# Kernel optimization log

Hardware: AMD Instinct MI355X
Metric: run time of the kernel (lower is better)

## Reference

```python
import jax, jax.numpy as jnp
from jax import lax
import numpy as np

DECAY = 0.5   # LIF membrane leak factor
VTH = 1.0     # firing threshold


def _conv(x, w, stride, pad):
    # x: [B,C,H,W], w: [O,I,kh,kw]
    return lax.conv_general_dilated(
        x, w, (stride, stride), [(pad, pad), (pad, pad)],
        dimension_numbers=('NCHW', 'OIHW', 'NCHW'))


def _convT(x, w, b, stride=2, pad=1):
    # torch ConvTranspose2d(in,out,k,stride,pad): w is [Cin,Cout,k,k]
    k = w.shape[-1]
    wf = jnp.flip(w, (-2, -1)).transpose(1, 0, 2, 3)  # -> [Cout,Cin,k,k]
    y = lax.conv_general_dilated(
        x, wf, (1, 1), [(k - 1 - pad, k - 1 - pad)] * 2,
        lhs_dilation=(stride, stride),
        dimension_numbers=('NCHW', 'OIHW', 'NCHW'))
    return y + b[None, :, None, None]


def setup_inputs() -> dict:
    key = jax.random.key(0)
    ks = jax.random.split(key, 8)
    T, B = 16, 32
    x_seq = (jax.random.uniform(ks[0], (T, B, 1, 100, 368)) < 0.1).astype(jnp.float32)

    def p(k, shape, fan_in):
        return jax.random.normal(k, shape, jnp.float32) * (1.0 / np.sqrt(fan_in))

    return {
        'x_seq': x_seq,
        'w1': p(ks[1], (16, 1, 5, 5), 25),
        'w2': p(ks[2], (32, 16, 3, 3), 16 * 9),
        'wd': p(ks[3], (64, 32, 3, 3), 32 * 9),
        'bd': jnp.zeros((64,), jnp.float32),
        'wt1': p(ks[4], (64, 32, 4, 4), 64 * 16),
        'bt1': jnp.zeros((32,), jnp.float32),
        'wt2': p(ks[5], (32, 2, 4, 4), 32 * 16),
        'bt2': jnp.zeros((2,), jnp.float32),
        'actual_batch_size': 32,
    }


def reference(x_seq, w1, w2, wd, bd, wt1, bt1, wt2, bt2, actual_batch_size):
    B = x_seq.shape[1]
    dt = x_seq.dtype
    mem1 = jnp.zeros((B, 16, 50, 184), dt)
    mem2 = jnp.zeros((B, 32, 25, 92), dt)

    def step(carry, x):
        m1, m2 = carry
        # spiking conv layer 1: leaky integrate, fire, hard reset
        m1 = m1 * DECAY + _conv(x, w1, 2, 2)
        s1 = (m1 >= VTH).astype(dt)
        m1 = m1 * (1.0 - s1)
        # spiking conv layer 2 (return_dense -> membrane kept for decoder)
        m2 = m2 * DECAY + _conv(s1, w2, 2, 1)
        s2 = (m2 >= VTH).astype(dt)
        m2 = m2 * (1.0 - s2)
        return (m1, m2), None

    (mem1, mem2), _ = lax.scan(step, (mem1, mem2), x_seq)

    # dense CNN decoder on final membrane state
    h = jax.nn.relu(_conv(mem2, wd, 1, 1) + bd[None, :, None, None])   # [B,64,25,92]
    h = jax.nn.relu(_convT(h, wt1, bt1))                               # [B,32,50,184]
    out = jax.nn.softplus(_convT(h, wt2, bt2))                         # [B,2,100,368]
    inv_tau_c_pred = out[:, 0:1]
    alpha_pred = out[:, 1:2]
    return inv_tau_c_pred, alpha_pred
```

## Files before the change

kernel.cpp:

```cpp
#include <hip/hip_runtime.h>
#include <hip/hip_bf16.h>
#include <cstddef>


#define T_STEPS 16
#define NB 32
#define H0 100
#define W0 368
#define C1 16
#define H1 50
#define W1 184
#define C2 32
#define H2 25
#define W2 92
#define CD 64
#define WPR 6
#define SITES2 2300
#define SITES1 9200

using f32x16 = __attribute__((ext_vector_type(16))) float;
using s16x8  = __attribute__((ext_vector_type(8))) short;

__device__ inline unsigned short f2bf(float f) {
    union { float f; unsigned int u; } v; v.f = f;
    unsigned int r = v.u + 0x7fffu + ((v.u >> 16) & 1u);
    return (unsigned short)(r >> 16);
}
__device__ inline float bf2f(unsigned short u) {
    union { unsigned int u; float f; } v; v.u = ((unsigned int)u) << 16;
    return v.f;
}
__device__ inline unsigned int pk2(float a, float b) {
    return (unsigned int)f2bf(a) | ((unsigned int)f2bf(b) << 16);
}
__device__ inline s16x8 ld8(const void* p) { return *reinterpret_cast<const s16x8*>(p); }

__global__ __launch_bounds__(256) void k_pack(const float* __restrict__ x,
                                              unsigned long long* __restrict__ xb) {
    long long gid = (long long)blockIdx.x * blockDim.x + threadIdx.x;
    long long widx = gid >> 6;
    int lane = (int)(gid & 63);
    const long long NWORDS = (long long)T_STEPS * NB * H0 * WPR;
    if (widx >= NWORDS) return;
    int wcol = (int)(widx % WPR);
    long long rowid = widx / WPR;
    int y = (int)(rowid % H0);
    long long tb = rowid / H0;
    int col = wcol * 64 + lane;
    float v = 0.f;
    if (col < W0) v = x[(tb * H0 + y) * W0 + col];
    unsigned long long mask = __ballot(v != 0.f);
    if (lane == 0) xb[widx] = mask;
}

__global__ __launch_bounds__(256) void k_snn1(const unsigned long long* __restrict__ xb,
                                              const float* __restrict__ w1,
                                              unsigned short* __restrict__ s1m) {
    __shared__ float sw[25 * C1];
    for (int i = threadIdx.x; i < 25 * C1; i += blockDim.x) {
        int k = i >> 4, c = i & 15;
        sw[i] = w1[c * 25 + k];
    }
    __syncthreads();

    int idx = blockIdx.x * blockDim.x + threadIdx.x;
    const int NPOS = NB * H1 * W1;
    if (idx >= NPOS) return;
    int x1 = idx % W1;
    int tmp = idx / W1;
    int y1 = tmp % H1;
    int b  = tmp / H1;

    float m1[C1];
#pragma unroll
    for (int c = 0; c < C1; ++c) m1[c] = 0.f;

    const int iy0 = 2 * y1 - 2;
    const int ix0 = 2 * x1 - 2;
    const int wi = ix0 >> 6;
    const int s  = ix0 & 63;

    for (int t = 0; t < T_STEPS; ++t) {
#pragma unroll
        for (int c = 0; c < C1; ++c) m1[c] *= 0.5f;

        const unsigned long long* xp = xb + ((size_t)(t * NB + b) * H0) * WPR;
        unsigned int bits25 = 0;
#pragma unroll
        for (int ky = 0; ky < 5; ++ky) {
            int iy = iy0 + ky;
            if (iy < 0 || iy >= H0) continue;
            const unsigned long long* row = xp + (size_t)iy * WPR;
            unsigned long long a = (wi >= 0) ? row[wi] : 0ull;
            unsigned long long bw = (wi + 1 < WPR) ? row[wi + 1] : 0ull;
            unsigned long long chunk = a >> s;
            if (s) chunk |= (bw << (64 - s));
            bits25 |= ((unsigned int)chunk & 31u) << (5 * ky);
        }
        while (bits25) {
            int k = __ffs(bits25) - 1;
            bits25 &= bits25 - 1;
            const float* wk = &sw[k * C1];
#pragma unroll
            for (int c = 0; c < C1; ++c) m1[c] += wk[c];
        }
        unsigned int mask = 0;
#pragma unroll
        for (int c = 0; c < C1; ++c) {
            if (m1[c] >= 1.0f) { mask |= (1u << c); m1[c] = 0.f; }
        }
        s1m[(size_t)t * NPOS + idx] = (unsigned short)mask;
    }
}

__global__ __launch_bounds__(256) void k_snn2(const unsigned short* __restrict__ s1m,
                                              const float* __restrict__ w2,
                                              unsigned short* __restrict__ mem2bf) {
    __shared__ float sw[9 * C1 * 36];
    for (int i = threadIdx.x; i < 9 * C1 * C2; i += blockDim.x) {
        int c2 = i & 31;
        int r = i >> 5;
        int ci = r & 15;
        int pos = r >> 4;
        sw[r * 36 + c2] = w2[(c2 * C1 + ci) * 9 + pos];
    }
    __syncthreads();

    int idx = blockIdx.x * blockDim.x + threadIdx.x;
    const int NPOS = NB * H2 * W2;
    if (idx >= NPOS) return;
    int x2 = idx % W2;
    int tmp = idx / W2;
    int y2 = tmp % H2;
    int b  = tmp / H2;

    float m2[C2];
#pragma unroll
    for (int c = 0; c < C2; ++c) m2[c] = 0.f;

    const int S1POS = NB * H1 * W1;
    for (int t = 0; t < T_STEPS; ++t) {
#pragma unroll
        for (int c = 0; c < C2; ++c) m2[c] *= 0.5f;
        const unsigned short* spk = s1m + (size_t)t * S1POS + (size_t)b * (H1 * W1);
#pragma unroll
        for (int ky = 0; ky < 3; ++ky) {
            int iy = 2 * y2 + ky - 1;
            if (iy < 0 || iy >= H1) continue;
#pragma unroll
            for (int kx = 0; kx < 3; ++kx) {
                int ix = 2 * x2 + kx - 1;
                if (ix < 0 || ix >= W1) continue;
                unsigned int mask = spk[iy * W1 + ix];
                while (mask) {
                    int ci = __ffs(mask) - 1;
                    mask &= mask - 1;
                    const float* wrow = &sw[((ky * 3 + kx) * C1 + ci) * 36];
#pragma unroll
                    for (int c = 0; c < C2; ++c) m2[c] += wrow[c];
                }
            }
        }
#pragma unroll
        for (int c = 0; c < C2; ++c) {
            if (m2[c] >= 1.0f) m2[c] = 0.f;
        }
    }
    size_t sbase = ((size_t)b * SITES2 + (size_t)y2 * W2 + x2) * C2;
    uint4* dst = (uint4*)(mem2bf + sbase);
#pragma unroll
    for (int g = 0; g < 4; ++g) {
        uint4 u;
        u.x = pk2(m2[g * 8 + 0], m2[g * 8 + 1]);
        u.y = pk2(m2[g * 8 + 2], m2[g * 8 + 3]);
        u.z = pk2(m2[g * 8 + 4], m2[g * 8 + 5]);
        u.w = pk2(m2[g * 8 + 6], m2[g * 8 + 7]);
        dst[g] = u;
    }
}

__global__ __launch_bounds__(256) void k_repackb(const float* __restrict__ wd,
                                                 const float* __restrict__ wt1,
                                                 const float* __restrict__ wt2,
                                                 unsigned short* __restrict__ wdb,
                                                 unsigned short* __restrict__ wt1b,
                                                 float* __restrict__ wt2k) {
    int gid = blockIdx.x * blockDim.x + threadIdx.x;
    if (gid < 64 * 288) {
        int co = gid / 288, k = gid % 288;
        int tap = k >> 5, ci = k & 31;
        wdb[gid] = f2bf(wd[((size_t)co * C2 + ci) * 9 + tap]);
    } else if (gid < 64 * 288 + 4 * 32 * 256) {
        int j = gid - 64 * 288;
        int par = j >> 13, co = (j >> 8) & 31, k = j & 255;
        int tap = k >> 6, ci = k & 63;
        int ty = tap >> 1, tx = tap & 1;
        int ry = par >> 1, rx = par & 1;
        int ky = ry ? (ty ? 0 : 2) : (ty ? 3 : 1);
        int kx = rx ? (tx ? 0 : 2) : (tx ? 3 : 1);
        wt1b[j] = f2bf(wt1[(((size_t)ci * 32 + co) * 4 + ky) * 4 + kx]);
    } else if (gid < 64 * 288 + 4 * 32 * 256 + 1024) {
        int j = gid - (64 * 288 + 4 * 32 * 256);
        int par = j >> 8, tap = (j >> 6) & 3, ci = (j >> 1) & 31, co = j & 1;
        int ty = tap >> 1, tx = tap & 1;
        int ry = par >> 1, rx = par & 1;
        int ky = ry ? (ty ? 0 : 2) : (ty ? 3 : 1);
        int kx = rx ? (tx ? 0 : 2) : (tx ? 3 : 1);
        wt2k[j] = wt2[(((size_t)ci * 2 + co) * 4 + ky) * 4 + kx];
    }
}

__global__ __launch_bounds__(256) void k_convd(const unsigned short* __restrict__ mem2bf,
                                               const unsigned short* __restrict__ wdb,
                                               const float* __restrict__ bd,
                                               unsigned short* __restrict__ h1bf) {
    int wave = threadIdx.x >> 6;
    int lane = threadIdx.x & 63;
    int col = lane & 31, hi = lane >> 5;
    int b = blockIdx.z;
    int n0 = (blockIdx.x * 4 + wave) * 32;
    int site = n0 + col;
    bool sval = site < SITES2;
    int sc = sval ? site : 0;
    int yy = sc / W2, xx = sc % W2;

    const char* ibase = (const char*)(mem2bf + (size_t)b * SITES2 * C2);
    int toff[9];
    bool tval[9];
#pragma unroll
    for (int ky = 0; ky < 3; ++ky)
#pragma unroll
        for (int kx = 0; kx < 3; ++kx) {
            int iy = yy + ky - 1, ix = xx + kx - 1;
            bool v = sval && iy >= 0 && iy < H2 && ix >= 0 && ix < W2;
            tval[ky * 3 + kx] = v;
            toff[ky * 3 + kx] = (iy * W2 + ix) * (C2 * 2);
        }

    const char* abase = (const char*)wdb;
    f32x16 acc0 = {}, acc1 = {};
    const s16x8 zero = {0, 0, 0, 0, 0, 0, 0, 0};
#pragma unroll
    for (int s = 0; s < 18; ++s) {
        int tap = s >> 1;
        int boff = (s & 1) * 32 + hi * 16;
        s16x8 bf = tval[tap] ? ld8(ibase + toff[tap] + boff) : zero;
        s16x8 a0 = ld8(abase + col * 576 + s * 32 + hi * 16);
        s16x8 a1 = ld8(abase + (col + 32) * 576 + s * 32 + hi * 16);
        acc0 = __builtin_amdgcn_mfma_f32_32x32x16_bf16(a0, bf, acc0, 0, 0, 0);
        acc1 = __builtin_amdgcn_mfma_f32_32x32x16_bf16(a1, bf, acc1, 0, 0, 0);
    }
    if (!sval) return;
    char* obase = (char*)(h1bf + ((size_t)b * SITES2 + site) * CD);
#pragma unroll
    for (int t = 0; t < 2; ++t) {
        const f32x16& ac = t ? acc1 : acc0;
#pragma unroll
        for (int q = 0; q < 4; ++q) {
            int co = t * 32 + 8 * q + 4 * hi;
            float v0 = fmaxf(ac[4 * q + 0] + bd[co + 0], 0.f);
            float v1 = fmaxf(ac[4 * q + 1] + bd[co + 1], 0.f);
            float v2 = fmaxf(ac[4 * q + 2] + bd[co + 2], 0.f);
            float v3 = fmaxf(ac[4 * q + 3] + bd[co + 3], 0.f);
            uint2 u; u.x = pk2(v0, v1); u.y = pk2(v2, v3);
            *(uint2*)(obase + co * 2) = u;
        }
    }
}

__global__ __launch_bounds__(256) void k_convt1(const unsigned short* __restrict__ h1bf,
                                                const unsigned short* __restrict__ wt1b,
                                                const float* __restrict__ bt1,
                                                unsigned short* __restrict__ h2bf) {
    int wave = threadIdx.x >> 6;
    int lane = threadIdx.x & 63;
    int col = lane & 31, hi = lane >> 5;
    int par = blockIdx.y;
    int ry = par >> 1, rx = par & 1;
    int b = blockIdx.z;
    int n0 = (blockIdx.x * 4 + wave) * 64;

    const char* ibase = (const char*)(h1bf + (size_t)b * SITES2 * CD);
    int toff[2][4];
    bool tval[2][4];
    int mm[2], nn[2];
    bool sv[2];
#pragma unroll
    for (int j = 0; j < 2; ++j) {
        int site = n0 + j * 32 + col;
        sv[j] = site < SITES2;
        int sc = sv[j] ? site : 0;
        int m = sc / W2, n = sc % W2;
        mm[j] = m; nn[j] = n;
        int iy1 = m + (ry ? 1 : -1);
        int ix1 = n + (rx ? 1 : -1);
        bool y1v = iy1 >= 0 && iy1 < H2;
        bool x1v = ix1 >= 0 && ix1 < W2;
#pragma unroll
        for (int t = 0; t < 4; ++t) {
            int ty = t >> 1, tx = t & 1;
            int iy = ty ? iy1 : m;
            int ix = tx ? ix1 : n;
            tval[j][t] = sv[j] && (ty ? y1v : true) && (tx ? x1v : true);
            toff[j][t] = (iy * W2 + ix) * (CD * 2);
        }
    }

    const char* abase = (const char*)(wt1b + (size_t)par * 32 * 256);
    f32x16 acc0 = {}, acc1 = {};
    const s16x8 zero = {0, 0, 0, 0, 0, 0, 0, 0};
#pragma unroll
    for (int s = 0; s < 16; ++s) {
        int tap = s >> 2;
        int boff = (s & 3) * 32 + hi * 16;
        s16x8 b0 = tval[0][tap] ? ld8(ibase + toff[0][tap] + boff) : zero;
        s16x8 b1 = tval[1][tap] ? ld8(ibase + toff[1][tap] + boff) : zero;
        s16x8 a = ld8(abase + col * 512 + s * 32 + hi * 16);
        acc0 = __builtin_amdgcn_mfma_f32_32x32x16_bf16(a, b0, acc0, 0, 0, 0);
        acc1 = __builtin_amdgcn_mfma_f32_32x32x16_bf16(a, b1, acc1, 0, 0, 0);
    }
#pragma unroll
    for (int j = 0; j < 2; ++j) {
        if (!sv[j]) continue;
        const f32x16& ac = j ? acc1 : acc0;
        int oy = 2 * mm[j] + ry, ox = 2 * nn[j] + rx;
        char* obase = (char*)(h2bf + ((size_t)b * SITES1 + (size_t)oy * W1 + ox) * C2);
#pragma unroll
        for (int q = 0; q < 4; ++q) {
            int co = 8 * q + 4 * hi;
            float v0 = fmaxf(ac[4 * q + 0] + bt1[co + 0], 0.f);
            float v1 = fmaxf(ac[4 * q + 1] + bt1[co + 1], 0.f);
            float v2 = fmaxf(ac[4 * q + 2] + bt1[co + 2], 0.f);
            float v3 = fmaxf(ac[4 * q + 3] + bt1[co + 3], 0.f);
            uint2 u; u.x = pk2(v0, v1); u.y = pk2(v2, v3);
            *(uint2*)(obase + co * 2) = u;
        }
    }
}

__global__ __launch_bounds__(256) void k_convt2(const unsigned short* __restrict__ h2bf,
                                                const float* __restrict__ wt2k,
                                                const float* __restrict__ bt2,
                                                float* __restrict__ out) {
    int i = blockIdx.x * blockDim.x + threadIdx.x;
    if (i >= SITES1) return;
    int par = blockIdx.y;
    int ry = par >> 1, rx = par & 1;
    int b = blockIdx.z;
    int m = i / W1, n = i % W1;
    int iy1 = m + (ry ? 1 : -1);
    int ix1 = n + (rx ? 1 : -1);
    bool y1v = iy1 >= 0 && iy1 < H1;
    bool x1v = ix1 >= 0 && ix1 < W1;

    float a0 = bt2[0], a1 = bt2[1];
    const unsigned short* ib = h2bf + (size_t)b * SITES1 * C2;
#pragma unroll
    for (int t = 0; t < 4; ++t) {
        int ty = t >> 1, tx = t & 1;
        if ((ty && !y1v) || (tx && !x1v)) continue;
        int iy = ty ? iy1 : m;
        int ix = tx ? ix1 : n;
        const unsigned short* p = ib + ((size_t)iy * W1 + ix) * C2;
        const float* w = wt2k + ((size_t)par * 4 + t) * 64;
#pragma unroll
        for (int g = 0; g < 4; ++g) {
            s16x8 v8 = ld8(p + g * 8);
#pragma unroll
            for (int e = 0; e < 8; ++e) {
                float v = bf2f((unsigned short)v8[e]);
                int ci = g * 8 + e;
                a0 += v * w[2 * ci];
                a1 += v * w[2 * ci + 1];
            }
        }
    }
    int oy = 2 * m + ry, ox = 2 * n + rx;
    size_t base_o = (size_t)b * (H0 * W0) + (size_t)oy * W0 + ox;
    out[base_o] = fmaxf(a0, 0.f) + log1pf(expf(-fabsf(a0)));
    out[(size_t)NB * H0 * W0 + base_o] = fmaxf(a1, 0.f) + log1pf(expf(-fabsf(a1)));
}

extern "C" void kernel_launch(void* const* d_in, const int* in_sizes, int n_in,
                              void* d_out, int out_size, void* d_ws, size_t ws_size,
                              hipStream_t stream) {
    const float* x   = (const float*)d_in[0];
    const float* w1  = (const float*)d_in[1];
    const float* w2  = (const float*)d_in[2];
    const float* wd  = (const float*)d_in[3];
    const float* bd  = (const float*)d_in[4];
    const float* wt1 = (const float*)d_in[5];
    const float* bt1 = (const float*)d_in[6];
    const float* wt2 = (const float*)d_in[7];
    const float* bt2 = (const float*)d_in[8];
    float* out = (float*)d_out;

    char* ws = (char*)d_ws;
    unsigned short* s1m    = (unsigned short*)(ws);
    unsigned short* mem2bf = (unsigned short*)(ws + 9420800);
    unsigned short* h1bf   = (unsigned short*)(ws + 14131200);
    unsigned short* h2bf   = (unsigned short*)(ws + 23552000);
    unsigned long long* xb = (unsigned long long*)(ws + 42393600);
    unsigned short* wdb    = (unsigned short*)(ws + 44851200);
    unsigned short* wt1b   = (unsigned short*)(ws + 44888064);
    float* wt2k            = (float*)(ws + 44953600);

    {
        long long nthreads = (long long)T_STEPS * NB * H0 * WPR * 64;
        int blocks = (int)((nthreads + 255) / 256);
        k_pack<<<blocks, 256, 0, stream>>>(x, xb);
    }
    {
        int n = NB * H1 * W1;
        k_snn1<<<(n + 255) / 256, 256, 0, stream>>>(xb, w1, s1m);
    }
    {
        int n = NB * H2 * W2;
        k_snn2<<<(n + 255) / 256, 256, 0, stream>>>(s1m, w2, mem2bf);
    }
    {
        int n = 64 * 288 + 4 * 32 * 256 + 1024;
        k_repackb<<<(n + 255) / 256, 256, 0, stream>>>(wd, wt1, wt2, wdb, wt1b, wt2k);
    }
    {
        dim3 g(18, 1, NB);
        k_convd<<<g, 256, 0, stream>>>(mem2bf, wdb, bd, h1bf);
    }
    {
        dim3 g(9, 4, NB);
        k_convt1<<<g, 256, 0, stream>>>(h1bf, wt1b, bt1, h2bf);
    }
    {
        dim3 g(36, 4, NB);
        k_convt2<<<g, 256, 0, stream>>>(h2bf, wt2k, bt2, out);
    }
}
```

Baseline: 230.7 us.

## Run SNN layer-2 spiking conv on MFMA with bf16x3 split weights and spike LUT

Replaces the per-thread sparse scalar accumulation in the second spiking conv layer with MFMA 32x32x16 bf16 matrix ops. Each 32-site tile's spike bitmasks are expanded into bf16 0/1 operands through a shared-memory lookup table. To keep fp32-level accuracy, the weights are split into three bf16 parts (hi, mid, lo) in the repack kernel, which now runs first. The membrane state stays in MFMA accumulators across timesteps. This trades the data-dependent bit-scan loops for dense matrix work, at the cost of 27 MFMAs per timestep and some rounding risk near the threshold.

```diff
diff --git a/kernel.cpp b/kernel.cpp
--- a/kernel.cpp
+++ b/kernel.cpp
@@ -114,77 +114,96 @@
 }
 
 __global__ __launch_bounds__(256) void k_snn2(const unsigned short* __restrict__ s1m,
-                                              const float* __restrict__ w2,
+                                              const unsigned short* __restrict__ w2b3,
                                               unsigned short* __restrict__ mem2bf) {
-    __shared__ float sw[9 * C1 * 36];
-    for (int i = threadIdx.x; i < 9 * C1 * C2; i += blockDim.x) {
-        int c2 = i & 31;
-        int r = i >> 5;
-        int ci = r & 15;
-        int pos = r >> 4;
-        sw[r * 36 + c2] = w2[(c2 * C1 + ci) * 9 + pos];
+    __shared__ uint4 lut[256];
+    {
+        int m = (int)threadIdx.x;
+        unsigned int wv[4];
+#pragma unroll
+        for (int h = 0; h < 4; ++h) {
+            unsigned int lo = (m >> (2 * h)) & 1u, hb = (m >> (2 * h + 1)) & 1u;
+            wv[h] = (lo ? 0x3F80u : 0u) | (hb ? 0x3F800000u : 0u);
+        }
+        lut[m] = make_uint4(wv[0], wv[1], wv[2], wv[3]);
     }
     __syncthreads();
 
-    int idx = blockIdx.x * blockDim.x + threadIdx.x;
-    const int NPOS = NB * H2 * W2;
-    if (idx >= NPOS) return;
-    int x2 = idx % W2;
-    int tmp = idx / W2;
-    int y2 = tmp % H2;
-    int b  = tmp / H2;
-
-    float m2[C2];
-#pragma unroll
-    for (int c = 0; c < C2; ++c) m2[c] = 0.f;
-
-    const int S1POS = NB * H1 * W1;
+    int wave = threadIdx.x >> 6;
+    int lane = threadIdx.x & 63;
+    int col = lane & 31, hi = lane >> 5;
+    int gsite = (blockIdx.x * 4 + wave) * 32 + col;
+    int b = gsite / SITES2;
+    int rest = gsite % SITES2;
+    int y2 = rest / W2, x2 = rest % W2;
+
+    int toff[9]; bool tval[9];
+#pragma unroll
+    for (int ky = 0; ky < 3; ++ky)
+#pragma unroll
+        for (int kx = 0; kx < 3; ++kx) {
+            int iy = 2 * y2 + ky - 1, ix = 2 * x2 + kx - 1;
+            tval[ky * 3 + kx] = iy >= 0 && iy < H1 && ix >= 0 && ix < W1;
+            toff[ky * 3 + kx] = iy * W1 + ix;
+        }
+
+    const char* ab = (const char*)w2b3;
+    s16x8 a0[9], a1[9], a2[9];
+#pragma unroll
+    for (int s = 0; s < 9; ++s) {
+        int ko = (s * 16 + hi * 8) * 2;
+        a0[s] = ld8(ab + (col * 144) * 2 + ko);
+        a1[s] = ld8(ab + ((32 + col) * 144) * 2 + ko);
+        a2[s] = ld8(ab + ((64 + col) * 144) * 2 + ko);
+    }
+
+    f32x16 acc = {};
+    int hsh = hi * 8;
+
     for (int t = 0; t < T_STEPS; ++t) {
-#pragma unroll
-        for (int c = 0; c < C2; ++c) m2[c] *= 0.5f;
-        const unsigned short* spk = s1m + (size_t)t * S1POS + (size_t)b * (H1 * W1);
-#pragma unroll
-        for (int ky = 0; ky < 3; ++ky) {
-            int iy = 2 * y2 + ky - 1;
-            if (iy < 0 || iy >= H1) continue;
-#pragma unroll
-            for (int kx = 0; kx < 3; ++kx) {
-                int ix = 2 * x2 + kx - 1;
-                if (ix < 0 || ix >= W1) continue;
-                unsigned int mask = spk[iy * W1 + ix];
-                while (mask) {
-                    int ci = __ffs(mask) - 1;
-                    mask &= mask - 1;
-                    const float* wrow = &sw[((ky * 3 + kx) * C1 + ci) * 36];
-#pragma unroll
-                    for (int c = 0; c < C2; ++c) m2[c] += wrow[c];
-                }
-            }
-        }
-#pragma unroll
-        for (int c = 0; c < C2; ++c) {
-            if (m2[c] >= 1.0f) m2[c] = 0.f;
-        }
-    }
-    size_t sbase = ((size_t)b * SITES2 + (size_t)y2 * W2 + x2) * C2;
-    uint4* dst = (uint4*)(mem2bf + sbase);
-#pragma unroll
-    for (int g = 0; g < 4; ++g) {
-        uint4 u;
-        u.x = pk2(m2[g * 8 + 0], m2[g * 8 + 1]);
-        u.y = pk2(m2[g * 8 + 2], m2[g * 8 + 3]);
-        u.z = pk2(m2[g * 8 + 4], m2[g * 8 + 5]);
-        u.w = pk2(m2[g * 8 + 6], m2[g * 8 + 7]);
-        dst[g] = u;
+        const unsigned short* spk = s1m + (size_t)t * (NB * H1 * W1) + (size_t)b * (H1 * W1);
+        unsigned int msk[9];
+#pragma unroll
+        for (int i = 0; i < 9; ++i)
+            msk[i] = tval[i] ? (unsigned int)spk[toff[i]] : 0u;
+
+#pragma unroll
+        for (int e = 0; e < 16; ++e) acc[e] *= 0.5f;
+
+#pragma unroll
+        for (int s = 0; s < 9; ++s) {
+            unsigned int byte = (msk[s] >> hsh) & 0xFFu;
+            s16x8 bf = *reinterpret_cast<const s16x8*>(&lut[byte]);
+            acc = __builtin_amdgcn_mfma_f32_32x32x16_bf16(a0[s], bf, acc, 0, 0, 0);
+            acc = __builtin_amdgcn_mfma_f32_32x32x16_bf16(a1[s], bf, acc, 0, 0, 0);
+            acc = __builtin_amdgcn_mfma_f32_32x32x16_bf16(a2[s], bf, acc, 0, 0, 0);
+        }
+#pragma unroll
+        for (int e = 0; e < 16; ++e) {
+            float v = acc[e];
+            acc[e] = (v >= 1.0f) ? 0.f : v;
+        }
+    }
+
+    char* obase = (char*)(mem2bf + (size_t)gsite * C2);
+#pragma unroll
+    for (int q = 0; q < 4; ++q) {
+        int co = 8 * q + 4 * hi;
+        uint2 u;
+        u.x = pk2(acc[4 * q + 0], acc[4 * q + 1]);
+        u.y = pk2(acc[4 * q + 2], acc[4 * q + 3]);
+        *(uint2*)(obase + co * 2) = u;
     }
 }
 
 __global__ __launch_bounds__(256) void k_repackb(const float* __restrict__ wd,
                                                  const float* __restrict__ wt1,
                                                  const float* __restrict__ wt2,
+                                                 const float* __restrict__ w2,
                                                  unsigned short* __restrict__ wdb,
                                                  unsigned short* __restrict__ wt1b,
-                                                 float* __restrict__ wt2k) {
+                                                 float* __restrict__ wt2k,
+                                                 unsigned short* __restrict__ w2b3) {
     int gid = blockIdx.x * blockDim.x + threadIdx.x;
     if (gid < 64 * 288) {
         int co = gid / 288, k = gid % 288;
@@ -207,6 +226,18 @@
         int ky = ry ? (ty ? 0 : 2) : (ty ? 3 : 1);
         int kx = rx ? (tx ? 0 : 2) : (tx ? 3 : 1);
         wt2k[j] = wt2[(((size_t)ci * 2 + co) * 4 + ky) * 4 + kx];
+    } else if (gid < 64 * 288 + 4 * 32 * 256 + 1024 + 3 * 32 * 144) {
+        int j = gid - (64 * 288 + 4 * 32 * 256 + 1024);
+        int p = j / 4608, rem = j % 4608;
+        int co = rem / 144, k = rem % 144;
+        int tap = k / 16, ci = k % 16;
+        float w = w2[((size_t)co * C1 + ci) * 9 + tap];
+        unsigned short b0 = f2bf(w);
+        float r1 = w - bf2f(b0);
+        unsigned short b1 = f2bf(r1);
+        float r2 = r1 - bf2f(b1);
+        unsigned short b2 = f2bf(r2);
+        w2b3[j] = (p == 0) ? b0 : (p == 1) ? b1 : b2;
     }
 }
 
@@ -404,7 +435,12 @@
     unsigned short* wdb    = (unsigned short*)(ws + 44851200);
     unsigned short* wt1b   = (unsigned short*)(ws + 44888064);
     float* wt2k            = (float*)(ws + 44953600);
-
+    unsigned short* w2b3   = (unsigned short*)(ws + 44957696);
+
+    {
+        int n = 64 * 288 + 4 * 32 * 256 + 1024 + 3 * 32 * 144;
+        k_repackb<<<(n + 255) / 256, 256, 0, stream>>>(wd, wt1, wt2, w2, wdb, wt1b, wt2k, w2b3);
+    }
     {
         long long nthreads = (long long)T_STEPS * NB * H0 * WPR * 64;
         int blocks = (int)((nthreads + 255) / 256);
@@ -415,12 +451,7 @@
         k_snn1<<<(n + 255) / 256, 256, 0, stream>>>(xb, w1, s1m);
     }
     {
-        int n = NB * H2 * W2;
-        k_snn2<<<(n + 255) / 256, 256, 0, stream>>>(s1m, w2, mem2bf);
-    }
-    {
-        int n = 64 * 288 + 4 * 32 * 256 + 1024;
-        k_repackb<<<(n + 255) / 256, 256, 0, stream>>>(wd, wt1, wt2, wdb, wt1b, wt2k);
+        k_snn2<<<575, 256, 0, stream>>>(s1m, w2b3, mem2bf);
     }
     {
         dim3 g(18, 1, NB);
```

New measurement: 207.4 us. 10.1% less time.
